# Kernel optimization log

Measured on AMD Instinct MI355X. Metric: run time of the kernel, lower is better.

## Reference

```python
import jax, jax.numpy as jnp
import numpy as np

B, S, D_IN, D_K, D_V = 4, 2048, 1024, 1024, 1024


def setup_inputs() -> dict:
    key = jax.random.key(0)
    ks = jax.random.split(key, 7)
    s_in = 1.0 / np.sqrt(D_IN)
    return {
        "x": jax.random.normal(ks[0], (B, S, D_IN), dtype=jnp.float32),
        "Wq": jax.random.uniform(ks[1], (D_K, D_IN), jnp.float32, -s_in, s_in),
        "bq": jax.random.uniform(ks[2], (D_K,), jnp.float32, -s_in, s_in),
        "Wk": jax.random.uniform(ks[3], (D_K, D_IN), jnp.float32, -s_in, s_in),
        "bk": jax.random.uniform(ks[4], (D_K,), jnp.float32, -s_in, s_in),
        "Wv": jax.random.uniform(ks[5], (D_V, D_IN), jnp.float32, -s_in, s_in),
        "bv": jax.random.uniform(ks[6], (D_V,), jnp.float32, -s_in, s_in),
    }


def reference(x, Wq, bq, Wk, bk, Wv, bv):
    # Linear: y = x @ W^T + b (torch convention, weight is [out, in])
    Q = jnp.einsum("bsd,kd->bsk", x, Wq) + bq  # [B,S,Dk]
    K = jnp.einsum("bsd,kd->bsk", x, Wk) + bk  # [B,S,Dk]
    V = jnp.einsum("bsd,vd->bsv", x, Wv) + bv  # [B,S,Dv]
    norm_fact = 1.0 / np.sqrt(D_K)
    # NOTE: faithful to original — softmax on raw scores, THEN scale by 1/sqrt(dim_k)
    scores = jnp.einsum("bqk,bsk->bqs", Q, K)          # [B,S,S]
    atten = jax.nn.softmax(scores, axis=-1) * norm_fact  # post-softmax scaling
    return jnp.einsum("bqs,bsv->bqv", atten, V)          # [B,S,Dv]
```

## Files before the change

### kernel.cpp

```cpp
#include <hip/hip_runtime.h>
#include <hip/hip_bf16.h>
#include <cstdint>
#include <cstddef>


typedef __attribute__((ext_vector_type(8))) _Float16 f16x8;
typedef __attribute__((ext_vector_type(4))) _Float16 f16x4;
typedef __attribute__((ext_vector_type(4))) float f32x4;

#define BM 128
#define BN 128
#define BK 64

#define NBATCH 4
#define SEQ 2048
#define DIM 1024
#define MTOT (NBATCH * SEQ)

__device__ __forceinline__ void async_ld16(const void* g, void* l) {
  __builtin_amdgcn_global_load_lds((__attribute__((address_space(1))) void*)(g),
                                   (__attribute__((address_space(3))) void*)(l),
                                   16, 0, 0);
}

__device__ __forceinline__ void gemm_core(const _Float16* __restrict__ A, int lda,
                                          const _Float16* __restrict__ B, int ldb,
                                          int K, int m0, int n0,
                                          _Float16* As, _Float16* Bs,
                                          f32x4 (&acc)[4][4]) {
  const int t = threadIdx.x;
  const int w = t >> 6;
  const int lrow = t & 15;
  const int quad = (t >> 4) & 3;
  const int wm = (w >> 1) << 6;
  const int wn = (w & 1) << 6;

  const int rb = t >> 3;
  const int co = (((t & 7) ^ (rb & 7)) << 3);
  const _Float16* Ap = A + (size_t)(m0 + rb) * lda + co;
  const _Float16* Bp = B + (size_t)(n0 + rb) * ldb + co;

  const int sw = lrow & 7;

  for (int k0 = 0; k0 < K; k0 += BK) {
#pragma unroll
    for (int i = 0; i < 4; ++i)
      async_ld16(Ap + (size_t)(i * 32) * lda + k0, As + i * 2048 + (w << 9));
#pragma unroll
    for (int i = 0; i < 4; ++i)
      async_ld16(Bp + (size_t)(i * 32) * ldb + k0, Bs + i * 2048 + (w << 9));
    __syncthreads();
#pragma unroll
    for (int kk = 0; kk < BK; kk += 32) {
      const int slot = ((kk >> 3) + quad) ^ sw;
      f16x8 af[4], bfr[4];
#pragma unroll
      for (int mi = 0; mi < 4; ++mi)
        af[mi] = *(const f16x8*)(As + (wm + mi * 16 + lrow) * BK + (slot << 3));
#pragma unroll
      for (int ni = 0; ni < 4; ++ni)
        bfr[ni] = *(const f16x8*)(Bs + (wn + ni * 16 + lrow) * BK + (slot << 3));
#pragma unroll
      for (int mi = 0; mi < 4; ++mi)
#pragma unroll
        for (int ni = 0; ni < 4; ++ni)
          acc[mi][ni] = __builtin_amdgcn_mfma_f32_16x16x32_f16(af[mi], bfr[ni],
                                                              acc[mi][ni], 0, 0, 0);
    }
    __syncthreads();
  }
}

__global__ __launch_bounds__(256) void split_all_kernel(
    const float* __restrict__ x, const float* __restrict__ Wq,
    const float* __restrict__ Wk, const float* __restrict__ Wv,
    _Float16* __restrict__ xh, _Float16* __restrict__ Wqh,
    _Float16* __restrict__ Wkh, _Float16* __restrict__ Wvh) {
  int r = blockIdx.x;
  const float* src;
  _Float16* dst;
  if (r < MTOT)            { src = x;  dst = xh;  }
  else if (r < MTOT + DIM) { src = Wq; dst = Wqh; r -= MTOT; }
  else if (r < MTOT + 2 * DIM) { src = Wk; dst = Wkh; r -= MTOT + DIM; }
  else                     { src = Wv; dst = Wvh; r -= MTOT + 2 * DIM; }
  const int t = threadIdx.x;
  const float4 v = ((const float4*)(src + (size_t)r * DIM))[t];
  f16x4 hi = {(_Float16)v.x, (_Float16)v.y, (_Float16)v.z, (_Float16)v.w};
  ((f16x4*)(dst + (size_t)r * DIM))[t] = hi;
}

__global__ __launch_bounds__(256, 2) void qkv_kernel(
    const _Float16* __restrict__ xh,
    const _Float16* __restrict__ Wqh, const float* __restrict__ bq,
    const _Float16* __restrict__ Wkh, const float* __restrict__ bk,
    const _Float16* __restrict__ Wvh, const float* __restrict__ bv,
    _Float16* __restrict__ Qp, _Float16* __restrict__ Kp,
    _Float16* __restrict__ Vt) {
  __shared__ alignas(16) _Float16 As[BM * BK];
  __shared__ alignas(16) _Float16 Bs[BN * BK];
  f32x4 acc[4][4] = {};
  const int l = blockIdx.x;
  const int z = l >> 9;
  const int r9 = l & 511;
  const int m0 = (((r9 & 7) | ((r9 >> 6) << 3))) * BM;
  const int n0 = ((r9 >> 3) & 7) * BN;
  const _Float16* W = (z == 0) ? Wqh : (z == 1) ? Wkh : Wvh;
  const float* bias = (z == 0) ? bq : (z == 1) ? bk : bv;
  gemm_core(xh, DIM, W, DIM, DIM, m0, n0, As, Bs, acc);

  const int t = threadIdx.x, w = t >> 6, lrow = t & 15, quad = (t >> 4) & 3;
  const int wm = (w >> 1) << 6, wn = (w & 1) << 6;
  if (z == 2) {
    const int b = m0 >> 11;
    const int s_base = (m0 & (SEQ - 1)) + wm + quad * 4;
#pragma unroll
    for (int ni = 0; ni < 4; ++ni) {
      const int col = n0 + wn + ni * 16 + lrow;
      const float bb = bias[col];
      _Float16* vrow = Vt + (size_t)((b << 10) + col) * SEQ;
#pragma unroll
      for (int mi = 0; mi < 4; ++mi) {
        f16x4 v4 = {(_Float16)(acc[mi][ni][0] + bb),
                    (_Float16)(acc[mi][ni][1] + bb),
                    (_Float16)(acc[mi][ni][2] + bb),
                    (_Float16)(acc[mi][ni][3] + bb)};
        *(f16x4*)(vrow + s_base + mi * 16) = v4;
      }
    }
  } else {
    _Float16* base = (z == 0) ? Qp : Kp;
#pragma unroll
    for (int ni = 0; ni < 4; ++ni) {
      const int col = n0 + wn + ni * 16 + lrow;
      const float bb = bias[col];
#pragma unroll
      for (int mi = 0; mi < 4; ++mi) {
#pragma unroll
        for (int r = 0; r < 4; ++r) {
          const int row = m0 + wm + mi * 16 + quad * 4 + r;
          base[(size_t)row * DIM + col] = (_Float16)(acc[mi][ni][r] + bb);
        }
      }
    }
  }
}

__global__ __launch_bounds__(256, 2) void scores_kernel(
    const _Float16* __restrict__ Qp, const _Float16* __restrict__ Kp,
    _Float16* __restrict__ Sc) {
  __shared__ alignas(16) _Float16 As[BM * BK];
  __shared__ alignas(16) _Float16 Bs[BN * BK];
  f32x4 acc[4][4] = {};
  const int l = blockIdx.x;
  const int b = l >> 8;
  const int r8 = l & 255;
  const int s = r8 >> 6;
  const int m0 = ((r8 & 7) | ((s & 1) << 3)) * BM;
  const int n0 = (((r8 >> 3) & 7) | ((s >> 1) << 3)) * BN;
  gemm_core(Qp + (size_t)b * SEQ * DIM, DIM,
            Kp + (size_t)b * SEQ * DIM, DIM, DIM, m0, n0, As, Bs, acc);
  _Float16* out = Sc + (size_t)b * SEQ * SEQ;
  const int t = threadIdx.x, w = t >> 6, lrow = t & 15, quad = (t >> 4) & 3;
  const int wm = (w >> 1) << 6, wn = (w & 1) << 6;
#pragma unroll
  for (int ni = 0; ni < 4; ++ni) {
    const int col = n0 + wn + ni * 16 + lrow;
#pragma unroll
    for (int mi = 0; mi < 4; ++mi) {
#pragma unroll
      for (int r = 0; r < 4; ++r) {
        const int row = m0 + wm + mi * 16 + quad * 4 + r;
        out[(size_t)row * SEQ + col] = (_Float16)acc[mi][ni][r];
      }
    }
  }
}

__global__ __launch_bounds__(256) void softmax_kernel(const _Float16* __restrict__ Sc,
                                                      _Float16* __restrict__ P) {
  const int r0 = blockIdx.x * 2;
  const _Float16* rowA = Sc + (size_t)r0 * SEQ;
  const _Float16* rowB = rowA + SEQ;
  _Float16* prowA = P + (size_t)r0 * SEQ;
  _Float16* prowB = prowA + SEQ;
  const int t = threadIdx.x;
  const int w = t >> 6;

  const f16x8 ha = ((const f16x8*)rowA)[t];
  const f16x8 hb = ((const f16x8*)rowB)[t];
  float a[8], bb[8];
#pragma unroll
  for (int j = 0; j < 8; ++j) { a[j] = (float)ha[j]; bb[j] = (float)hb[j]; }

  float mA = fmaxf(fmaxf(fmaxf(a[0], a[1]), fmaxf(a[2], a[3])),
                   fmaxf(fmaxf(a[4], a[5]), fmaxf(a[6], a[7])));
  float mB = fmaxf(fmaxf(fmaxf(bb[0], bb[1]), fmaxf(bb[2], bb[3])),
                   fmaxf(fmaxf(bb[4], bb[5]), fmaxf(bb[6], bb[7])));
#pragma unroll
  for (int o = 32; o; o >>= 1) {
    mA = fmaxf(mA, __shfl_down(mA, o));
    mB = fmaxf(mB, __shfl_down(mB, o));
  }
  __shared__ float red[16];
  if ((t & 63) == 0) { red[w] = mA; red[w + 4] = mB; }
  __syncthreads();
  mA = fmaxf(fmaxf(red[0], red[1]), fmaxf(red[2], red[3]));
  mB = fmaxf(fmaxf(red[4], red[5]), fmaxf(red[6], red[7]));

  float eA[8], eB[8];
#pragma unroll
  for (int j = 0; j < 8; ++j) {
    eA[j] = __expf(a[j] - mA);
    eB[j] = __expf(bb[j] - mB);
  }
  float sA = ((eA[0] + eA[1]) + (eA[2] + eA[3])) + ((eA[4] + eA[5]) + (eA[6] + eA[7]));
  float sB = ((eB[0] + eB[1]) + (eB[2] + eB[3])) + ((eB[4] + eB[5]) + (eB[6] + eB[7]));
#pragma unroll
  for (int o = 32; o; o >>= 1) {
    sA += __shfl_down(sA, o);
    sB += __shfl_down(sB, o);
  }
  if ((t & 63) == 0) { red[8 + w] = sA; red[12 + w] = sB; }
  __syncthreads();
  sA = (red[8] + red[9]) + (red[10] + red[11]);
  sB = (red[12] + red[13]) + (red[14] + red[15]);

  const float scA = 0.03125f / sA;
  const float scB = 0.03125f / sB;
  f16x8 oA, oB;
#pragma unroll
  for (int j = 0; j < 8; ++j) {
    oA[j] = (_Float16)(eA[j] * scA);
    oB[j] = (_Float16)(eB[j] * scB);
  }
  ((f16x8*)prowA)[t] = oA;
  ((f16x8*)prowB)[t] = oB;
}

__global__ __launch_bounds__(256, 2) void pv_kernel(
    const _Float16* __restrict__ P, const _Float16* __restrict__ Vt,
    float* __restrict__ out) {
  __shared__ alignas(16) _Float16 As[BM * BK];
  __shared__ alignas(16) _Float16 Bs[BN * BK];
  f32x4 acc[4][4] = {};
  const int l = blockIdx.x;
  const int b = l >> 7;
  const int r7 = l & 127;
  const int m0 = ((r7 & 7) | ((r7 >> 6) << 3)) * BM;
  const int n0 = ((r7 >> 3) & 7) * BN;
  gemm_core(P + (size_t)b * SEQ * SEQ, SEQ,
            Vt + (size_t)b * DIM * SEQ, SEQ, SEQ, m0, n0, As, Bs, acc);
  float* ob = out + (size_t)b * SEQ * DIM;
  const int t = threadIdx.x, w = t >> 6, lrow = t & 15, quad = (t >> 4) & 3;
  const int wm = (w >> 1) << 6, wn = (w & 1) << 6;
#pragma unroll
  for (int ni = 0; ni < 4; ++ni) {
    const int col = n0 + wn + ni * 16 + lrow;
#pragma unroll
    for (int mi = 0; mi < 4; ++mi) {
#pragma unroll
      for (int r = 0; r < 4; ++r) {
        const int row = m0 + wm + mi * 16 + quad * 4 + r;
        ob[(size_t)row * DIM + col] = acc[mi][ni][r];
      }
    }
  }
}

extern "C" void kernel_launch(void* const* d_in, const int* in_sizes, int n_in,
                              void* d_out, int out_size, void* d_ws, size_t ws_size,
                              hipStream_t stream) {
  const float* x  = (const float*)d_in[0];
  const float* Wq = (const float*)d_in[1];
  const float* bq = (const float*)d_in[2];
  const float* Wk = (const float*)d_in[3];
  const float* bk = (const float*)d_in[4];
  const float* Wv = (const float*)d_in[5];
  const float* bv = (const float*)d_in[6];
  float* out = (float*)d_out;

  char* ws = (char*)d_ws;
  _Float16* Qp  = (_Float16*)(ws);
  _Float16* Kp  = (_Float16*)(ws + 16777216);
  _Float16* Vt  = (_Float16*)(ws + 33554432);
  _Float16* Sc  = (_Float16*)(ws + 50331648);
  _Float16* P   = (_Float16*)(ws + 117440512);
  _Float16* xh  = (_Float16*)(ws + 50331648);
  _Float16* Wqh = (_Float16*)(ws + 67108864);
  _Float16* Wkh = (_Float16*)(ws + 69206016);
  _Float16* Wvh = (_Float16*)(ws + 71303168);

  dim3 blk(256, 1, 1);
  split_all_kernel<<<dim3(MTOT + 3 * DIM), blk, 0, stream>>>(
      x, Wq, Wk, Wv, xh, Wqh, Wkh, Wvh);
  qkv_kernel<<<dim3(3 * 512), blk, 0, stream>>>(
      xh, Wqh, bq, Wkh, bk, Wvh, bv, Qp, Kp, Vt);
  scores_kernel<<<dim3(NBATCH * 256), blk, 0, stream>>>(Qp, Kp, Sc);
  softmax_kernel<<<dim3(MTOT / 2), blk, 0, stream>>>(Sc, P);
  pv_kernel<<<dim3(NBATCH * 128), blk, 0, stream>>>(P, Vt, out);
}
```

Baseline: 236.5 us.

## Rewrite scores GEMM with 256x256 tiles, 8 waves, double-buffered swizzled LDS

The Q·K^T scores kernel now uses 256x256 output tiles per 512-thread block, with 8 waves each owning a 128x64 sub-tile. It double-buffers LDS with XOR-swizzled layouts and interleaves async global-to-LDS prefetch of the next K-slice between four MFMA phases, using sched_barrier and setprio. The aim is more data reuse per load, fewer LDS bank conflicts, and load latency hidden behind compute. In exchange it uses 128KB of LDS and more accumulator registers, and launches only 256 blocks, which may underfill the CUs.

```diff
diff --git a/kernel.cpp b/kernel.cpp
--- a/kernel.cpp
+++ b/kernel.cpp
@@ -16,6 +16,8 @@
 #define SEQ 2048
 #define DIM 1024
 #define MTOT (NBATCH * SEQ)
+
+template <int Q> struct ic { static constexpr int val = Q; };
 
 __device__ __forceinline__ void async_ld16(const void* g, void* l) {
   __builtin_amdgcn_global_load_lds((__attribute__((address_space(1))) void*)(g),
@@ -145,32 +147,117 @@
   }
 }
 
-__global__ __launch_bounds__(256, 2) void scores_kernel(
+__global__ __launch_bounds__(512, 2) void scores_kernel(
     const _Float16* __restrict__ Qp, const _Float16* __restrict__ Kp,
     _Float16* __restrict__ Sc) {
-  __shared__ alignas(16) _Float16 As[BM * BK];
-  __shared__ alignas(16) _Float16 Bs[BN * BK];
-  f32x4 acc[4][4] = {};
+  __shared__ alignas(16) _Float16 sA[2][256 * 64];
+  __shared__ alignas(16) _Float16 sB[2][256 * 64];
   const int l = blockIdx.x;
-  const int b = l >> 8;
-  const int r8 = l & 255;
-  const int s = r8 >> 6;
-  const int m0 = ((r8 & 7) | ((s & 1) << 3)) * BM;
-  const int n0 = (((r8 >> 3) & 7) | ((s >> 1) << 3)) * BN;
-  gemm_core(Qp + (size_t)b * SEQ * DIM, DIM,
-            Kp + (size_t)b * SEQ * DIM, DIM, DIM, m0, n0, As, Bs, acc);
+  const int mt = l & 7;
+  const int i2 = l >> 3;
+  const int nt_ = i2 & 7;
+  const int b  = i2 >> 3;
+  const int m0 = mt * 256, n0 = nt_ * 256;
+  const _Float16* Ag = Qp + (size_t)b * SEQ * DIM;
+  const _Float16* Bg = Kp + (size_t)b * SEQ * DIM;
+
+  const int t = threadIdx.x;
+  const int w = t >> 6;
+  const int lrow = t & 15;
+  const int quad = (t >> 4) & 3;
+  const int wm = w >> 2;
+  const int wn = w & 3;
+  const int sw = lrow & 7;
+
+  const int rb = t >> 3;
+  const int co = (((t & 7) ^ (rb & 7)) << 3);
+  const _Float16* ApS = Ag + (size_t)(m0 + rb) * DIM + co;
+  const _Float16* BpS = Bg + (size_t)(n0 + rb) * DIM + co;
+  const int ldst = (w << 9);
+
+  f32x4 acc[8][4] = {};
+
+  auto stageA = [&](int buf, int hh, int k0) {
+#pragma unroll
+    for (int ii = 0; ii < 2; ++ii)
+      async_ld16(ApS + (size_t)(hh * 128 + ii * 64) * DIM + k0,
+                 &sA[buf][hh * 8192 + ii * 4096 + ldst]);
+  };
+  auto stageB = [&](int buf, int hh, int k0) {
+#pragma unroll
+    for (int ii = 0; ii < 2; ++ii)
+      async_ld16(BpS + (size_t)(hh * 128 + ii * 64) * DIM + k0,
+                 &sB[buf][hh * 8192 + ii * 4096 + ldst]);
+  };
+
+  auto phase = [&](int buf, auto qtag) {
+    constexpr int Qq = decltype(qtag)::val;
+    constexpr int qm = Qq & 1, qn = Qq >> 1;
+    f16x8 af[4][2], bf[2][2];
+#pragma unroll
+    for (int mi = 0; mi < 4; ++mi) {
+      const int rh = (qm * 4 + mi) * 16 + lrow;
+#pragma unroll
+      for (int k2 = 0; k2 < 2; ++k2) {
+        const int slot = ((k2 << 2) + quad) ^ sw;
+        af[mi][k2] = *(const f16x8*)&sA[buf][wm * 8192 + rh * 64 + (slot << 3)];
+      }
+    }
+#pragma unroll
+    for (int nj = 0; nj < 2; ++nj) {
+      const int rh = (wn & 1) * 64 + (qn * 2 + nj) * 16 + lrow;
+#pragma unroll
+      for (int k2 = 0; k2 < 2; ++k2) {
+        const int slot = ((k2 << 2) + quad) ^ sw;
+        bf[nj][k2] = *(const f16x8*)&sB[buf][(wn >> 1) * 8192 + rh * 64 + (slot << 3)];
+      }
+    }
+    __builtin_amdgcn_s_setprio(1);
+#pragma unroll
+    for (int mi = 0; mi < 4; ++mi)
+#pragma unroll
+      for (int nj = 0; nj < 2; ++nj)
+#pragma unroll
+        for (int k2 = 0; k2 < 2; ++k2)
+          acc[qm * 4 + mi][qn * 2 + nj] = __builtin_amdgcn_mfma_f32_16x16x32_f16(
+              af[mi][k2], bf[nj][k2], acc[qm * 4 + mi][qn * 2 + nj], 0, 0, 0);
+    __builtin_amdgcn_s_setprio(0);
+  };
+
+  stageA(0, 0, 0); stageA(0, 1, 0); stageB(0, 0, 0); stageB(0, 1, 0);
+  __syncthreads();
+
+  const int NT = DIM / 64;
+  int c = 0;
+  for (int tt = 0; tt < NT; ++tt) {
+    const int k1 = (tt + 1) * 64;
+    const bool pf = (tt + 1 < NT);
+    __builtin_amdgcn_sched_barrier(0);
+    if (pf) stageA(c ^ 1, 0, k1);
+    phase(c, ic<0>{});
+    __builtin_amdgcn_sched_barrier(0);
+    if (pf) stageA(c ^ 1, 1, k1);
+    phase(c, ic<1>{});
+    __builtin_amdgcn_sched_barrier(0);
+    if (pf) stageB(c ^ 1, 0, k1);
+    phase(c, ic<2>{});
+    __builtin_amdgcn_sched_barrier(0);
+    if (pf) stageB(c ^ 1, 1, k1);
+    phase(c, ic<3>{});
+    __syncthreads();
+    c ^= 1;
+  }
+
   _Float16* out = Sc + (size_t)b * SEQ * SEQ;
-  const int t = threadIdx.x, w = t >> 6, lrow = t & 15, quad = (t >> 4) & 3;
-  const int wm = (w >> 1) << 6, wn = (w & 1) << 6;
-#pragma unroll
-  for (int ni = 0; ni < 4; ++ni) {
-    const int col = n0 + wn + ni * 16 + lrow;
-#pragma unroll
-    for (int mi = 0; mi < 4; ++mi) {
+#pragma unroll
+  for (int fm = 0; fm < 8; ++fm) {
+#pragma unroll
+    for (int fn = 0; fn < 4; ++fn) {
+      const int col = n0 + wn * 64 + fn * 16 + lrow;
 #pragma unroll
       for (int r = 0; r < 4; ++r) {
-        const int row = m0 + wm + mi * 16 + quad * 4 + r;
-        out[(size_t)row * SEQ + col] = (_Float16)acc[mi][ni][r];
+        const int row = m0 + wm * 128 + fm * 16 + quad * 4 + r;
+        out[(size_t)row * SEQ + col] = (_Float16)acc[fm][fn][r];
       }
     }
   }
@@ -295,7 +382,7 @@
       x, Wq, Wk, Wv, xh, Wqh, Wkh, Wvh);
   qkv_kernel<<<dim3(3 * 512), blk, 0, stream>>>(
       xh, Wqh, bq, Wkh, bk, Wvh, bv, Qp, Kp, Vt);
-  scores_kernel<<<dim3(NBATCH * 256), blk, 0, stream>>>(Qp, Kp, Sc);
+  scores_kernel<<<dim3(256), dim3(512, 1, 1), 0, stream>>>(Qp, Kp, Sc);
   softmax_kernel<<<dim3(MTOT / 2), blk, 0, stream>>>(Sc, P);
   pv_kernel<<<dim3(NBATCH * 128), blk, 0, stream>>>(P, Vt, out);
 }
```

Result: slower. 246.8 us (+4.4%).

## Double-buffer LDS tiles in shared GEMM core to overlap loads with MFMA

Applied to the files above, without the earlier changes.

Adds a prologue that stages the first K-tile, then in each iteration issues the async global-to-LDS loads for the next tile into an alternate buffer before running the MFMAs on the current one. This removes one barrier per iteration and is meant to hide global load latency behind compute in the QKV, scores and PV GEMMs. LDS per block doubles to 64KB. With two blocks per CU that is 128KB, so occupancy may be tighter. Overlap also depends on the compiler not inserting conservative vmcnt waits before the LDS reads.

```diff
diff --git a/kernel.cpp b/kernel.cpp
--- a/kernel.cpp
+++ b/kernel.cpp
@@ -11,6 +11,7 @@
 #define BM 128
 #define BN 128
 #define BK 64
+#define TILE_H (BM * BK)
 
 #define NBATCH 4
 #define SEQ 2048
@@ -21,6 +22,17 @@
   __builtin_amdgcn_global_load_lds((__attribute__((address_space(1))) void*)(g),
                                    (__attribute__((address_space(3))) void*)(l),
                                    16, 0, 0);
+}
+
+__device__ __forceinline__ void stage_k(const _Float16* __restrict__ Ap, int lda,
+                                        const _Float16* __restrict__ Bp, int ldb,
+                                        int k0, _Float16* As, _Float16* Bs, int w) {
+#pragma unroll
+  for (int i = 0; i < 4; ++i)
+    async_ld16(Ap + (size_t)(i * 32) * lda + k0, As + i * 2048 + (w << 9));
+#pragma unroll
+  for (int i = 0; i < 4; ++i)
+    async_ld16(Bp + (size_t)(i * 32) * ldb + k0, Bs + i * 2048 + (w << 9));
 }
 
 __device__ __forceinline__ void gemm_core(const _Float16* __restrict__ A, int lda,
@@ -42,24 +54,27 @@
 
   const int sw = lrow & 7;
 
+  stage_k(Ap, lda, Bp, ldb, 0, As, Bs, w);
+  __syncthreads();
+
+  int buf = 0;
   for (int k0 = 0; k0 < K; k0 += BK) {
-#pragma unroll
-    for (int i = 0; i < 4; ++i)
-      async_ld16(Ap + (size_t)(i * 32) * lda + k0, As + i * 2048 + (w << 9));
-#pragma unroll
-    for (int i = 0; i < 4; ++i)
-      async_ld16(Bp + (size_t)(i * 32) * ldb + k0, Bs + i * 2048 + (w << 9));
-    __syncthreads();
+    const int nxt = k0 + BK;
+    if (nxt < K)
+      stage_k(Ap, lda, Bp, ldb, nxt, As + (buf ^ 1) * TILE_H,
+              Bs + (buf ^ 1) * TILE_H, w);
+    const _Float16* Ac = As + buf * TILE_H;
+    const _Float16* Bc = Bs + buf * TILE_H;
 #pragma unroll
     for (int kk = 0; kk < BK; kk += 32) {
       const int slot = ((kk >> 3) + quad) ^ sw;
       f16x8 af[4], bfr[4];
 #pragma unroll
       for (int mi = 0; mi < 4; ++mi)
-        af[mi] = *(const f16x8*)(As + (wm + mi * 16 + lrow) * BK + (slot << 3));
+        af[mi] = *(const f16x8*)(Ac + (wm + mi * 16 + lrow) * BK + (slot << 3));
 #pragma unroll
       for (int ni = 0; ni < 4; ++ni)
-        bfr[ni] = *(const f16x8*)(Bs + (wn + ni * 16 + lrow) * BK + (slot << 3));
+        bfr[ni] = *(const f16x8*)(Bc + (wn + ni * 16 + lrow) * BK + (slot << 3));
 #pragma unroll
       for (int mi = 0; mi < 4; ++mi)
 #pragma unroll
@@ -68,6 +83,7 @@
                                                               acc[mi][ni], 0, 0, 0);
     }
     __syncthreads();
+    buf ^= 1;
   }
 }
 
@@ -96,8 +112,8 @@
     const _Float16* __restrict__ Wvh, const float* __restrict__ bv,
     _Float16* __restrict__ Qp, _Float16* __restrict__ Kp,
     _Float16* __restrict__ Vt) {
-  __shared__ alignas(16) _Float16 As[BM * BK];
-  __shared__ alignas(16) _Float16 Bs[BN * BK];
+  __shared__ alignas(16) _Float16 As[2 * TILE_H];
+  __shared__ alignas(16) _Float16 Bs[2 * TILE_H];
   f32x4 acc[4][4] = {};
   const int l = blockIdx.x;
   const int z = l >> 9;
@@ -148,8 +164,8 @@
 __global__ __launch_bounds__(256, 2) void scores_kernel(
     const _Float16* __restrict__ Qp, const _Float16* __restrict__ Kp,
     _Float16* __restrict__ Sc) {
-  __shared__ alignas(16) _Float16 As[BM * BK];
-  __shared__ alignas(16) _Float16 Bs[BN * BK];
+  __shared__ alignas(16) _Float16 As[2 * TILE_H];
+  __shared__ alignas(16) _Float16 Bs[2 * TILE_H];
   f32x4 acc[4][4] = {};
   const int l = blockIdx.x;
   const int b = l >> 8;
@@ -240,8 +256,8 @@
 __global__ __launch_bounds__(256, 2) void pv_kernel(
     const _Float16* __restrict__ P, const _Float16* __restrict__ Vt,
     float* __restrict__ out) {
-  __shared__ alignas(16) _Float16 As[BM * BK];
-  __shared__ alignas(16) _Float16 Bs[BN * BK];
+  __shared__ alignas(16) _Float16 As[2 * TILE_H];
+  __shared__ alignas(16) _Float16 Bs[2 * TILE_H];
   f32x4 acc[4][4] = {};
   const int l = blockIdx.x;
   const int b = l >> 7;
```

Result: slower. 252.7 us (+6.9%).
